# Performance work log

Measured on AMD Instinct MI355X. Metric: run time of the kernel, lower is better.

Reference implementation:

```python
import jax, jax.numpy as jnp
import numpy as np

# Dimensions inferred from the module (few-shot reweighted YOLOv2 region loss)
B, C, NA, NCPA = 64, 20, 5, 1          # batch, base classes, anchors, classes-per-anchor
H, W = 19, 19                           # feature map (608 input / stride 32)
T = 50                                  # cfg.max_boxes
THRESH = 0.6
COORD_SCALE = 1.0
CLASS_SCALE = 1.0
NB = B * C                              # per-class 'image' rows, as in the torch code
A4 = NA * H * W
EPS = 1e-12
BCE_EPS = 1e-7
ANCHORS = [[1.3221, 1.73145], [3.19275, 4.00944], [5.05587, 8.09892], [9.47112, 4.84053], [11.2364, 10.0071]]


def iou_xywh(x1, y1, w1, h1, x2, y2, w2, h2):
    # center-size IoU, matches darknet bbox_iou(x1y1x2y2=False)
    l = jnp.maximum(x1 - w1 * 0.5, x2 - w2 * 0.5)
    r = jnp.minimum(x1 + w1 * 0.5, x2 + w2 * 0.5)
    t = jnp.maximum(y1 - h1 * 0.5, y2 - h2 * 0.5)
    b = jnp.minimum(y1 + h1 * 0.5, y2 + h2 * 0.5)
    inter = jnp.clip(r - l, 0.0) * jnp.clip(b - t, 0.0)
    union = w1 * h1 + w2 * h2 - inter
    return inter / jnp.maximum(union, EPS)


def setup_inputs() -> dict:
    key = jax.random.key(0)
    k1, k2, k3, k4 = jax.random.split(key, 4)
    output = jax.random.normal(k1, (NB, NA * (5 + NCPA), H, W), jnp.float32) * 0.5
    # target rows: [cls, x, y, w, h] * T, coords in (0,1); x kept > 0 so all boxes are 'valid'
    cls_ids = jax.random.randint(k2, (B, C, T), 0, C).astype(jnp.float32)
    xy = jax.random.uniform(k3, (B, C, T, 2), minval=0.05, maxval=0.95)
    wh = jax.random.uniform(k4, (B, C, T, 2), minval=0.05, maxval=0.5)
    target = jnp.concatenate([cls_ids[..., None], xy, wh], axis=-1).reshape(B, C, T * 5)
    anchors = jnp.asarray(ANCHORS, jnp.float32)
    return {"output": output, "target": target, "anchors": anchors}


def _forward(output, target, anchors):
    target = jax.lax.stop_gradient(target)
    anchors = jax.lax.stop_gradient(anchors)
    out5 = output.reshape(NB, NA, 5 + NCPA, H, W)
    x = jax.nn.sigmoid(out5[:, :, 0])
    y = jax.nn.sigmoid(out5[:, :, 1])
    w = out5[:, :, 2]
    h = out5[:, :, 3]
    conf = jax.nn.sigmoid(out5[:, :, 4])
    # class logits regrouped to original batch: (B*NA*H*W, C)
    cls = out5[:, :, 5:5 + NCPA].reshape(NB, NA, H, W)
    cls_logits = cls.reshape(B, C, NA * H * W).transpose(0, 2, 1).reshape(-1, C)
    # decode pred boxes (detached, mirroring torch's use of .data)
    grid_x = jnp.arange(W, dtype=jnp.float32)[None, None, None, :]
    grid_y = jnp.arange(H, dtype=jnp.float32)[None, None, :, None]
    aw = anchors[:, 0][None, :, None, None]
    ah = anchors[:, 1][None, :, None, None]
    px = jax.lax.stop_gradient(x) + grid_x
    py = jax.lax.stop_gradient(y) + grid_y
    pw = jnp.exp(jax.lax.stop_gradient(w)) * aw
    ph = jnp.exp(jax.lax.stop_gradient(h)) * ah
    # ground-truth boxes per row
    tgt = target.reshape(NB, T, 5)
    cls_t = tgt[:, :, 0]
    gx = tgt[:, :, 1] * W
    gy = tgt[:, :, 2] * H
    gw = tgt[:, :, 3] * W
    gh = tgt[:, :, 4] * H
    # 'break on first zero x' semantics
    valid = jnp.cumprod((tgt[:, :, 1] != 0).astype(jnp.int32), axis=1) > 0
    # stage 1: zero conf_mask where any gt IoU > thresh (scan over T to avoid (NB,T,A4) blowup)
    pxf = px.reshape(NB, A4); pyf = py.reshape(NB, A4)
    pwf = pw.reshape(NB, A4); phf = ph.reshape(NB, A4)

    def iou_step(ci, xs):
        gxt, gyt, gwt, ght, vt = xs
        iou = iou_xywh(pxf, pyf, pwf, phf, gxt[:, None], gyt[:, None], gwt[:, None], ght[:, None])
        return jnp.maximum(ci, jnp.where(vt[:, None], iou, 0.0)), None

    cur_ious, _ = jax.lax.scan(iou_step, jnp.zeros((NB, A4), jnp.float32), (gx.T, gy.T, gw.T, gh.T, valid.T))
    conf_mask0 = jnp.where(cur_ious.reshape(NB, NA, H, W) > THRESH, 0.0, 1.0)
    # best anchor per gt by wh-only IoU
    inter = jnp.minimum(gw[..., None], anchors[:, 0]) * jnp.minimum(gh[..., None], anchors[:, 1])
    union = gw[..., None] * gh[..., None] + anchors[:, 0] * anchors[:, 1] - inter
    best_n = jnp.argmax(inter / jnp.maximum(union, EPS), axis=-1).astype(jnp.int32)  # (NB,T)
    gi = gx.astype(jnp.int32)
    gj = gy.astype(jnp.int32)
    # stage 2: ordered scatter of targets (later boxes overwrite earlier, as in the torch loops)
    binds = jnp.arange(NB)
    z = jnp.zeros((NB, NA, H, W), jnp.float32)
    # seen < 12800 branch: tx=ty=0.5, tw=th=0, coord_mask=1
    carry0 = (jnp.ones_like(z), z, conf_mask0, jnp.full_like(z, 0.5), jnp.full_like(z, 0.5), z, z, z, z)

    def tgt_step(carry, xs):
        cm, clm, cfm, tx, ty, tw, th, tconf, tcls = carry
        gxt, gyt, gwt, ght, bn, git, gjt, vt, ct = xs
        idx = (binds, bn, gjt, git)

        def upd(arr, val):
            return arr.at[idx].set(jnp.where(vt, val, arr[idx]))

        aw_b = anchors[bn, 0]
        ah_b = anchors[bn, 1]
        iou = iou_xywh(gxt, gyt, gwt, ght, px[idx], py[idx], pw[idx], ph[idx])
        cm = upd(cm, 1.0)
        clm = upd(clm, 1.0)
        cfm = upd(cfm, 1.0)
        tx = upd(tx, gxt - git.astype(jnp.float32))
        ty = upd(ty, gyt - gjt.astype(jnp.float32))
        tw = upd(tw, jnp.log(jnp.maximum(gwt, EPS) / aw_b))
        th = upd(th, jnp.log(jnp.maximum(ght, EPS) / ah_b))
        tconf = upd(tconf, iou)
        tcls = upd(tcls, ct)
        return (cm, clm, cfm, tx, ty, tw, th, tconf, tcls), None

    xs = (gx.T, gy.T, gw.T, gh.T, best_n.T, gi.T, gj.T, valid.T, cls_t.T)
    (coord_mask, cls_mask, conf_mask, tx, ty, tw, th, tconf, tcls), _ = jax.lax.scan(tgt_step, carry0, xs)
    # regroup per-class rows back to original batch (neg_ratio='full' -> counts[i] == C)
    cm_grp = cls_mask.reshape(B, C, NA, H, W).sum(axis=1)
    tcls_grp = tcls.reshape(B, C, NA, H, W).sum(axis=1)
    sel = (cm_grp == 1.0).reshape(-1)           # exclude colliding cells
    labels = tcls_grp.reshape(-1).astype(jnp.int32)

    def bce_mean(p, t):
        p = jnp.clip(p, BCE_EPS, 1.0 - BCE_EPS)
        return jnp.mean(-(t * jnp.log(p) + (1.0 - t) * jnp.log(1.0 - p)))

    loss_x = COORD_SCALE * bce_mean(x * coord_mask, tx * coord_mask)
    loss_y = COORD_SCALE * bce_mean(y * coord_mask, ty * coord_mask)
    loss_w = COORD_SCALE * 0.5 * jnp.mean((w * coord_mask - tw * coord_mask) ** 2)
    loss_h = COORD_SCALE * 0.5 * jnp.mean((h * coord_mask - th * coord_mask) ** 2)
    loss_conf = 0.5 * jnp.mean((conf * conf_mask - tconf * conf_mask) ** 2)
    logp = jax.nn.log_softmax(cls_logits, axis=-1)
    nll = -jnp.take_along_axis(logp, labels[:, None], axis=1)[:, 0]
    nsel = jnp.maximum(jnp.sum(sel.astype(jnp.float32)), 1.0)
    loss_cls = CLASS_SCALE * jnp.sum(jnp.where(sel, nll, 0.0)) / nsel
    return loss_x + loss_y + loss_w + loss_h + loss_conf + loss_cls


def reference(output, target, anchors):
    return _forward(output, target, anchors)
```

## Files before the change

kernel.cpp:

```cpp
#include <hip/hip_runtime.h>
#include <math.h>

constexpr int cB   = 64;
constexpr int cC   = 20;
constexpr int cNA  = 5;
constexpr int cH   = 19;
constexpr int cW   = 19;
constexpr int cT   = 50;
constexpr int cNB  = cB * cC;
constexpr int cHW  = cH * cW;
constexpr int cA4  = cNA * cHW;
constexpr int cCH  = cNA * 6;
constexpr long cNTOT = (long)cNB * cA4;
constexpr int cCLS_ROWS = cB * cA4;
constexpr int cCLS_BLOCKS = (cCLS_ROWS + 255) / 256;

constexpr int ACC_BANKS = 64;
constexpr int TGT_N   = cNB * cT;
constexpr size_t SZT   = (size_t)TGT_N * 4;
constexpr size_t OFF_CNT = 2560;
constexpr size_t OFF_GX  = 4096;
constexpr size_t OFF_GY  = OFF_GX  + SZT;
constexpr size_t OFF_GW  = OFF_GY  + SZT;
constexpr size_t OFF_GH  = OFF_GW  + SZT;
constexpr size_t OFF_CLS = OFF_GH  + SZT;
constexpr size_t OFF_HL  = OFF_CLS + SZT;
constexpr size_t OFF_HR  = OFF_HL  + SZT;
constexpr size_t OFF_HT  = OFF_HR  + SZT;
constexpr size_t OFF_HB  = OFF_HT  + SZT;
constexpr size_t OFF_HG  = OFF_HB  + SZT;
constexpr size_t OFF_WIN = OFF_HG  + SZT;

__device__ __forceinline__ float fexp(float x) {
    return __builtin_amdgcn_exp2f(x * 1.4426950408889634f);
}
__device__ __forceinline__ float flog(float x) {
    return __builtin_amdgcn_logf(x) * 0.6931471805599453f;
}
__device__ __forceinline__ float frcp(float x) { return __builtin_amdgcn_rcpf(x); }
__device__ __forceinline__ float fsigmoid(float x) { return frcp(1.0f + fexp(-x)); }

typedef _Float16 h2 __attribute__((ext_vector_type(2)));
union HU { unsigned u; h2 h; };
__device__ __forceinline__ unsigned splat2(float v) {
    HU x; _Float16 f = (_Float16)v; x.h[0] = f; x.h[1] = f; return x.u;
}

__global__ void k_prep(const float* __restrict__ target, const float* __restrict__ anch,
                       float* __restrict__ gx_, float* __restrict__ gy_,
                       float* __restrict__ gw_, float* __restrict__ gh_,
                       float* __restrict__ cls_,
                       unsigned* __restrict__ hl_, unsigned* __restrict__ hr_,
                       unsigned* __restrict__ ht_, unsigned* __restrict__ hb_,
                       unsigned* __restrict__ hg_,
                       int* __restrict__ winner, double* __restrict__ acc,
                       int* __restrict__ cnt) {
    const int nb = blockIdx.x;
    const int t  = threadIdx.x;
    if (nb == 0) {
        for (int k = t; k < 5 * ACC_BANKS; k += 64) acc[k] = 0.0;
        if (t == 0) *cnt = 0;
    }
    for (int k = t; k < cA4; k += 64) winner[(size_t)nb * cA4 + k] = -1;

    float cv = 0.f, xr = 1.f, yr = 0.f, wr = 0.f, hr = 0.f;
    if (t < cT) {
        const float* tg = target + (size_t)nb * (cT * 5) + t * 5;
        cv = tg[0]; xr = tg[1]; yr = tg[2]; wr = tg[3]; hr = tg[4];
    }
    unsigned long long nz = __ballot(xr != 0.0f);
    if (t < cT) {
        unsigned long long below = (t == 63) ? ~0ull : ((2ull << t) - 1ull);
        bool valid = ((~nz) & below) == 0ull;
        float gx = xr * (float)cW, gy = yr * (float)cH;
        float gw = wr * (float)cW, gh = hr * (float)cH;
        int o = nb * cT + t;
        gx_[o] = gx; gy_[o] = gy; gw_[o] = gw; gh_[o] = gh;
        cls_[o] = cv;
        if (valid) {
            hl_[o] = splat2(gx - 0.5f * gw);
            hr_[o] = splat2(gx + 0.5f * gw);
            ht_[o] = splat2(gy - 0.5f * gh);
            hb_[o] = splat2(gy + 0.5f * gh);
            hg_[o] = splat2(-0.6f * (gw * gh));
        } else {
            hl_[o] = splat2(1e30f);  hr_[o] = splat2(-1e30f);
            ht_[o] = splat2(1e30f);  hb_[o] = splat2(-1e30f);
            hg_[o] = splat2(0.0f);
        }
        float best = -1.0f; int bn = 0;
        for (int n = 0; n < cNA; ++n) {
            float aw = anch[2*n], ah = anch[2*n+1];
            float inter = fminf(gw, aw) * fminf(gh, ah);
            float uni   = gw*gh + aw*ah - inter;
            float r = inter / fmaxf(uni, 1e-12f);
            if (r > best) { best = r; bn = n; }
        }
        if (valid) {
            int gi = (int)gx, gj = (int)gy;
            atomicMax(&winner[(size_t)nb * cA4 + bn * cHW + gj * cW + gi], t);
        }
    }
    __syncthreads();
}

__launch_bounds__(256)
__global__ void k_main(const float* __restrict__ outp, const float* __restrict__ anch,
                       const float* __restrict__ gx_, const float* __restrict__ gy_,
                       const float* __restrict__ gw_, const float* __restrict__ gh_,
                       const unsigned* __restrict__ hl_, const unsigned* __restrict__ hr_,
                       const unsigned* __restrict__ ht_, const unsigned* __restrict__ hb_,
                       const unsigned* __restrict__ hg_,
                       const int* __restrict__ winner, double* __restrict__ acc) {
    __shared__ double s_red[3][4];
    const int tid  = threadIdx.x;
    const int nb   = blockIdx.x >> 1;
    const int base = ((blockIdx.x & 1) << 10) + tid;
    const int tb   = nb * cT;
    const float* obase = outp + (size_t)nb * (cCH * cHW);

    h2 pl2[2], pr2[2], pt2[2], pb2[2], ov2[2], pa06h[2];
    float conf[4], tcf[4];
    unsigned wbits = 0;
    float bce = 0.0f, sq = 0.0f;
    const h2 z2  = { (_Float16)0.0f, (_Float16)0.0f };
    const h2 c16 = { (_Float16)1.6f, (_Float16)1.6f };

    #pragma unroll
    for (int u = 0; u < 4; ++u) {
        int cell = base + (u << 8);
        bool a_  = cell < cA4;
        int cc   = a_ ? cell : (cA4 - 1);
        int na   = cc / cHW;
        int rem  = cc - na * cHW;
        int j    = rem / cW;
        int i    = rem - j * cW;
        const float* ob = obase + (size_t)(na * 6) * cHW + rem;
        float xl = ob[0], yl = ob[cHW], wl = ob[2*cHW], hl = ob[3*cHW], cl = ob[4*cHW];
        float aw = anch[2*na], ah = anch[2*na+1];
        float x  = fsigmoid(xl), y = fsigmoid(yl), cf = fsigmoid(cl);
        float px = x + (float)i, py = y + (float)j;
        float pw = fexp(wl) * aw, ph = fexp(hl) * ah;
        float l0 = px - 0.5f*pw, r0 = px + 0.5f*pw;
        float t0 = py - 0.5f*ph, b0 = py + 0.5f*ph;
        float pa = pw * ph;
        int p = u >> 1, s = u & 1;
        pl2[p][s] = (_Float16)l0;  pr2[p][s] = (_Float16)r0;
        pt2[p][s] = (_Float16)t0;  pb2[p][s] = (_Float16)b0;
        pa06h[p][s] = (_Float16)(0.6f * pa);
        ov2[p][s] = (_Float16)0.0f;
        conf[u] = cf; tcf[u] = 0.0f;

        float tx = 0.5f, ty = 0.5f, tw = 0.0f, th = 0.0f;
        int wt = winner[(size_t)nb * cA4 + cc];
        bool wfl = (wt >= 0) && a_;
        if (wfl) {
            wbits |= (1u << u);
            float gx = gx_[tb+wt], gy = gy_[tb+wt], gw = gw_[tb+wt], gh = gh_[tb+wt];
            tx = gx - (float)i; ty = gy - (float)j;
            tw = flog(fmaxf(gw, 1e-12f) * frcp(aw));
            th = flog(fmaxf(gh, 1e-12f) * frcp(ah));
            float iw = fminf(r0, gx + 0.5f*gw) - fmaxf(l0, gx - 0.5f*gw);
            float ih = fminf(b0, gy + 0.5f*gh) - fmaxf(t0, gy - 0.5f*gh);
            iw = fmaxf(iw, 0.0f); ih = fmaxf(ih, 0.0f);
            float inter = iw * ih;
            float uni   = gw*gh + pa - inter;
            tcf[u] = inter * frcp(fmaxf(uni, 1e-12f));
        }
        if (a_) {
            float pc = fminf(fmaxf(x, 1e-7f), 1.0f - 1e-7f);
            bce += -(tx * flog(pc) + (1.0f - tx) * flog(1.0f - pc));
            pc = fminf(fmaxf(y, 1e-7f), 1.0f - 1e-7f);
            bce += -(ty * flog(pc) + (1.0f - ty) * flog(1.0f - pc));
            float dw = wl - tw, dh = hl - th;
            sq += dw*dw + dh*dh;
        }
    }

    #pragma unroll 10
    for (int t = 0; t < cT; ++t) {
        HU a, b, c, d, e;
        a.u = hl_[tb + t]; b.u = hr_[tb + t];
        c.u = ht_[tb + t]; d.u = hb_[tb + t];
        e.u = hg_[tb + t];
        #pragma unroll
        for (int p = 0; p < 2; ++p) {
            h2 iw = __builtin_elementwise_min(pr2[p], b.h) - __builtin_elementwise_max(pl2[p], a.h);
            h2 ih = __builtin_elementwise_min(pb2[p], d.h) - __builtin_elementwise_max(pt2[p], c.h);
            iw = __builtin_elementwise_max(iw, z2);
            ih = __builtin_elementwise_max(ih, z2);
            ov2[p] = __builtin_elementwise_max(ov2[p], c16 * iw * ih + e.h);
        }
    }

    float sc = 0.0f;
    #pragma unroll
    for (int u = 0; u < 4; ++u) {
        int cell = base + (u << 8);
        if (cell >= cA4) continue;
        int p = u >> 1, s = u & 1;
        bool wfl  = (wbits >> u) & 1;
        bool over = ov2[p][s] > pa06h[p][s];
        float cm  = wfl ? 1.0f : (over ? 0.0f : 1.0f);
        float d   = (conf[u] - tcf[u]) * cm;
        sc += d * d;
    }

    double v0 = (double)bce, v1 = (double)sq, v2 = (double)sc;
    for (int off = 32; off > 0; off >>= 1) {
        v0 += __shfl_down(v0, off);
        v1 += __shfl_down(v1, off);
        v2 += __shfl_down(v2, off);
    }
    int lane = tid & 63, wid = tid >> 6;
    if (lane == 0) { s_red[0][wid] = v0; s_red[1][wid] = v1; s_red[2][wid] = v2; }
    __syncthreads();
    if (tid == 0) {
        double a0 = s_red[0][0] + s_red[0][1] + s_red[0][2] + s_red[0][3];
        double a1 = s_red[1][0] + s_red[1][1] + s_red[1][2] + s_red[1][3];
        double a2 = s_red[2][0] + s_red[2][1] + s_red[2][2] + s_red[2][3];
        int bank = blockIdx.x & (ACC_BANKS - 1);
        atomicAdd(&acc[0*ACC_BANKS + bank], a0);
        atomicAdd(&acc[1*ACC_BANKS + bank], a1);
        atomicAdd(&acc[2*ACC_BANKS + bank], a2);
    }
}

__launch_bounds__(256)
__global__ void k_cls(const float* __restrict__ outp, const float* __restrict__ cls_,
                      const int* __restrict__ winner, double* __restrict__ acc,
                      int* __restrict__ cnt, float* __restrict__ out) {
    __shared__ double s_red[2][4];
    __shared__ int s_last;
    int tid = threadIdx.x;
    int row = blockIdx.x * 256 + tid;
    double nll = 0.0, ns = 0.0;
    if (row < cCLS_ROWS) {
        int b = row / cA4;
        int a = row - b * cA4;
        int cnt1 = 0, selc = -1, selw = -1;
        #pragma unroll
        for (int c = 0; c < cC; ++c) {
            int wv = winner[(size_t)(b * cC + c) * cA4 + a];
            if (wv >= 0) { cnt1++; selc = c; selw = wv; }
        }
        if (cnt1 == 1) {
            int na  = a / cHW;
            int rem = a - na * cHW;
            const float* ob = outp + ((size_t)b * cC * cCH + na * 6 + 5) * cHW + rem;
            float l[cC]; float m = -1e30f;
            #pragma unroll
            for (int c = 0; c < cC; ++c) { l[c] = ob[(size_t)c * cCH * cHW]; m = fmaxf(m, l[c]); }
            float s = 0.0f;
            #pragma unroll
            for (int c = 0; c < cC; ++c) s += fexp(l[c] - m);
            int label = (int)cls_[(b * cC + selc) * cT + selw];
            nll = (double)(m + flog(s) - l[label]);
            ns  = 1.0;
        }
    }
    for (int off = 32; off > 0; off >>= 1) {
        nll += __shfl_down(nll, off);
        ns  += __shfl_down(ns, off);
    }
    int lane = tid & 63, wid = tid >> 6;
    if (lane == 0) { s_red[0][wid] = nll; s_red[1][wid] = ns; }
    __syncthreads();
    if (tid == 0) {
        double a0 = s_red[0][0] + s_red[0][1] + s_red[0][2] + s_red[0][3];
        double a1 = s_red[1][0] + s_red[1][1] + s_red[1][2] + s_red[1][3];
        int bank = blockIdx.x & (ACC_BANKS - 1);
        atomicAdd(&acc[3*ACC_BANKS + bank], a0);
        atomicAdd(&acc[4*ACC_BANKS + bank], a1);
        __threadfence();
        s_last = (atomicAdd(cnt, 1) == cCLS_BLOCKS - 1);
    }
    __syncthreads();
    if (s_last && tid < 64) {
        __threadfence();
        double s[5];
        #pragma unroll
        for (int j = 0; j < 5; ++j) {
            double v = atomicAdd(&acc[j * ACC_BANKS + tid], 0.0);
            for (int off = 32; off > 0; off >>= 1) v += __shfl_down(v, off);
            s[j] = v;
        }
        if (tid == 0) {
            double Ninv = 1.0 / (double)cNTOT;
            double loss = s[0] * Ninv
                        + 0.5 * s[1] * Ninv
                        + 0.5 * s[2] * Ninv
                        + s[3] / fmax(s[4], 1.0);
            out[0] = (float)loss;
        }
    }
}

extern "C" void kernel_launch(void* const* d_in, const int* in_sizes, int n_in,
                              void* d_out, int out_size, void* d_ws, size_t ws_size,
                              hipStream_t stream) {
    const float* output = (const float*)d_in[0];
    const float* target = (const float*)d_in[1];
    const float* anch   = (const float*)d_in[2];
    char* ws = (char*)d_ws;
    double*   acc  = (double*)ws;
    int*      cnt  = (int*)   (ws + OFF_CNT);
    float*    gx_  = (float*) (ws + OFF_GX);
    float*    gy_  = (float*) (ws + OFF_GY);
    float*    gw_  = (float*) (ws + OFF_GW);
    float*    gh_  = (float*) (ws + OFF_GH);
    float*    cls_ = (float*) (ws + OFF_CLS);
    unsigned* hl_  = (unsigned*)(ws + OFF_HL);
    unsigned* hr_  = (unsigned*)(ws + OFF_HR);
    unsigned* ht_  = (unsigned*)(ws + OFF_HT);
    unsigned* hb_  = (unsigned*)(ws + OFF_HB);
    unsigned* hg_  = (unsigned*)(ws + OFF_HG);
    int*      win  = (int*)   (ws + OFF_WIN);

    k_prep<<<cNB, 64, 0, stream>>>(target, anch, gx_, gy_, gw_, gh_, cls_,
                                   hl_, hr_, ht_, hb_, hg_, win, acc, cnt);
    k_main<<<cNB * 2, 256, 0, stream>>>(output, anch, gx_, gy_, gw_, gh_,
                                        hl_, hr_, ht_, hb_, hg_, win, acc);
    k_cls<<<cCLS_BLOCKS, 256, 0, stream>>>(output, cls_, win, acc, cnt, (float*)d_out);
}
```

Before: 141.3 us.

## Fuse target prep into main kernel with shared-memory winners and packed row encoding

Drops the separate prep kernel. Each main block now builds its ground-truth boxes and the winner map in shared memory, and processes one whole class-image (8 cells per thread) instead of half of one. Winning cells are packed into a per-batch row-encoding array with atomicAdd (count in the high bits, class and target index in the low bits). The class kernel therefore reads one int per row instead of 20 winner entries. This removes a launch and the global winner, box and gt arrays, at the cost of a memset, larger per-block work (half as many blocks) and more register pressure. The fp16 overlap check is rescaled by sqrt(1.6) instead of multiplying by 1.6.

```diff
diff --git a/kernel.cpp b/kernel.cpp
--- a/kernel.cpp
+++ b/kernel.cpp
@@ -16,20 +16,9 @@
 constexpr int cCLS_BLOCKS = (cCLS_ROWS + 255) / 256;
 
 constexpr int ACC_BANKS = 64;
-constexpr int TGT_N   = cNB * cT;
-constexpr size_t SZT   = (size_t)TGT_N * 4;
 constexpr size_t OFF_CNT = 2560;
-constexpr size_t OFF_GX  = 4096;
-constexpr size_t OFF_GY  = OFF_GX  + SZT;
-constexpr size_t OFF_GW  = OFF_GY  + SZT;
-constexpr size_t OFF_GH  = OFF_GW  + SZT;
-constexpr size_t OFF_CLS = OFF_GH  + SZT;
-constexpr size_t OFF_HL  = OFF_CLS + SZT;
-constexpr size_t OFF_HR  = OFF_HL  + SZT;
-constexpr size_t OFF_HT  = OFF_HR  + SZT;
-constexpr size_t OFF_HB  = OFF_HT  + SZT;
-constexpr size_t OFF_HG  = OFF_HB  + SZT;
-constexpr size_t OFF_WIN = OFF_HG  + SZT;
+constexpr size_t OFF_ROW = 4096;
+constexpr size_t ZERO_BYTES = OFF_ROW + (size_t)cB * cA4 * 4;
 
 __device__ __forceinline__ float fexp(float x) {
     return __builtin_amdgcn_exp2f(x * 1.4426950408889634f);
@@ -45,90 +34,94 @@
 __device__ __forceinline__ unsigned splat2(float v) {
     HU x; _Float16 f = (_Float16)v; x.h[0] = f; x.h[1] = f; return x.u;
 }
-
-__global__ void k_prep(const float* __restrict__ target, const float* __restrict__ anch,
-                       float* __restrict__ gx_, float* __restrict__ gy_,
-                       float* __restrict__ gw_, float* __restrict__ gh_,
-                       float* __restrict__ cls_,
-                       unsigned* __restrict__ hl_, unsigned* __restrict__ hr_,
-                       unsigned* __restrict__ ht_, unsigned* __restrict__ hb_,
-                       unsigned* __restrict__ hg_,
-                       int* __restrict__ winner, double* __restrict__ acc,
-                       int* __restrict__ cnt) {
-    const int nb = blockIdx.x;
-    const int t  = threadIdx.x;
-    if (nb == 0) {
-        for (int k = t; k < 5 * ACC_BANKS; k += 64) acc[k] = 0.0;
-        if (t == 0) *cnt = 0;
-    }
-    for (int k = t; k < cA4; k += 64) winner[(size_t)nb * cA4 + k] = -1;
-
-    float cv = 0.f, xr = 1.f, yr = 0.f, wr = 0.f, hr = 0.f;
-    if (t < cT) {
-        const float* tg = target + (size_t)nb * (cT * 5) + t * 5;
-        cv = tg[0]; xr = tg[1]; yr = tg[2]; wr = tg[3]; hr = tg[4];
-    }
-    unsigned long long nz = __ballot(xr != 0.0f);
-    if (t < cT) {
-        unsigned long long below = (t == 63) ? ~0ull : ((2ull << t) - 1ull);
-        bool valid = ((~nz) & below) == 0ull;
-        float gx = xr * (float)cW, gy = yr * (float)cH;
-        float gw = wr * (float)cW, gh = hr * (float)cH;
-        int o = nb * cT + t;
-        gx_[o] = gx; gy_[o] = gy; gw_[o] = gw; gh_[o] = gh;
-        cls_[o] = cv;
+constexpr float cS = 1.2649110640673518f;
+
+__launch_bounds__(256)
+__global__ void k_main(const float* __restrict__ outp, const float* __restrict__ target,
+                       const float* __restrict__ anch,
+                       int* __restrict__ rowenc, double* __restrict__ acc) {
+    __shared__ int s_win[cA4];
+    __shared__ __align__(16) unsigned s_box[cT][8];
+    __shared__ __align__(16) float4 s_gt[cT];
+    __shared__ double s_red[3][4];
+    const int tid = threadIdx.x;
+    const int nb  = blockIdx.x;
+    const int b_  = nb / cC;
+    const int c_  = nb - b_ * cC;
+    const float* obase = outp + (size_t)nb * (cCH * cHW);
+
+    for (int k = tid; k < cA4; k += 256) s_win[k] = -1;
+    __syncthreads();
+
+    if (tid < 64) {
+        const int t = tid;
+        float cv = 0.f, xr = 1.f, yr = 0.f, wr = 0.f, hr = 0.f;
+        if (t < cT) {
+            const float* tg = target + (size_t)nb * (cT * 5) + t * 5;
+            cv = tg[0]; xr = tg[1]; yr = tg[2]; wr = tg[3]; hr = tg[4];
+        }
+        (void)cv;
+        unsigned long long nz = __ballot(xr != 0.0f);
+        if (t < cT) {
+            unsigned long long below = (2ull << t) - 1ull;
+            bool valid = ((~nz) & below) == 0ull;
+            float gx = xr * (float)cW, gy = yr * (float)cH;
+            float gw = wr * (float)cW, gh = hr * (float)cH;
+            s_gt[t] = make_float4(gx, gy, gw, gh);
+            if (valid) {
+                s_box[t][0] = splat2(cS * (gx - 0.5f * gw));
+                s_box[t][1] = splat2(cS * (gx + 0.5f * gw));
+                s_box[t][2] = splat2(cS * (gy - 0.5f * gh));
+                s_box[t][3] = splat2(cS * (gy + 0.5f * gh));
+                s_box[t][4] = splat2(-0.6f * (gw * gh));
+            } else {
+                s_box[t][0] = splat2(1e4f);  s_box[t][1] = splat2(-1e4f);
+                s_box[t][2] = splat2(1e4f);  s_box[t][3] = splat2(-1e4f);
+                s_box[t][4] = splat2(0.0f);
+            }
+            if (valid) {
+                float best = -1.0f; int bn = 0;
+                for (int n = 0; n < cNA; ++n) {
+                    float aw = anch[2*n], ah = anch[2*n+1];
+                    float inter = fminf(gw, aw) * fminf(gh, ah);
+                    float uni   = gw*gh + aw*ah - inter;
+                    float r = inter / fmaxf(uni, 1e-12f);
+                    if (r > best) { best = r; bn = n; }
+                }
+                int cell = bn * cHW + (int)gy * cW + (int)gx;
+                atomicMax(&s_win[cell], t);
+            }
+        }
+    }
+    __syncthreads();
+    if (tid < cT) {
+        const float4 g = s_gt[tid];
+        HU hu; hu.u = s_box[tid][4];
+        bool valid = !((float)hu.h[0] == 0.0f && s_box[tid][1] == splat2(-1e4f));
         if (valid) {
-            hl_[o] = splat2(gx - 0.5f * gw);
-            hr_[o] = splat2(gx + 0.5f * gw);
-            ht_[o] = splat2(gy - 0.5f * gh);
-            hb_[o] = splat2(gy + 0.5f * gh);
-            hg_[o] = splat2(-0.6f * (gw * gh));
-        } else {
-            hl_[o] = splat2(1e30f);  hr_[o] = splat2(-1e30f);
-            ht_[o] = splat2(1e30f);  hb_[o] = splat2(-1e30f);
-            hg_[o] = splat2(0.0f);
-        }
-        float best = -1.0f; int bn = 0;
-        for (int n = 0; n < cNA; ++n) {
-            float aw = anch[2*n], ah = anch[2*n+1];
-            float inter = fminf(gw, aw) * fminf(gh, ah);
-            float uni   = gw*gh + aw*ah - inter;
-            float r = inter / fmaxf(uni, 1e-12f);
-            if (r > best) { best = r; bn = n; }
-        }
-        if (valid) {
-            int gi = (int)gx, gj = (int)gy;
-            atomicMax(&winner[(size_t)nb * cA4 + bn * cHW + gj * cW + gi], t);
-        }
-    }
-    __syncthreads();
-}
-
-__launch_bounds__(256)
-__global__ void k_main(const float* __restrict__ outp, const float* __restrict__ anch,
-                       const float* __restrict__ gx_, const float* __restrict__ gy_,
-                       const float* __restrict__ gw_, const float* __restrict__ gh_,
-                       const unsigned* __restrict__ hl_, const unsigned* __restrict__ hr_,
-                       const unsigned* __restrict__ ht_, const unsigned* __restrict__ hb_,
-                       const unsigned* __restrict__ hg_,
-                       const int* __restrict__ winner, double* __restrict__ acc) {
-    __shared__ double s_red[3][4];
-    const int tid  = threadIdx.x;
-    const int nb   = blockIdx.x >> 1;
-    const int base = ((blockIdx.x & 1) << 10) + tid;
-    const int tb   = nb * cT;
-    const float* obase = outp + (size_t)nb * (cCH * cHW);
-
-    h2 pl2[2], pr2[2], pt2[2], pb2[2], ov2[2], pa06h[2];
-    float conf[4], tcf[4];
+            float best = -1.0f; int bn = 0;
+            for (int n = 0; n < cNA; ++n) {
+                float aw = anch[2*n], ah = anch[2*n+1];
+                float inter = fminf(g.z, aw) * fminf(g.w, ah);
+                float uni   = g.z*g.w + aw*ah - inter;
+                float r = inter / fmaxf(uni, 1e-12f);
+                if (r > best) { best = r; bn = n; }
+            }
+            int cell = bn * cHW + (int)g.y * cW + (int)g.x;
+            if (s_win[cell] == tid)
+                atomicAdd(&rowenc[b_ * cA4 + cell], (1 << 10) | (c_ * cT + tid));
+        }
+    }
+
+    h2 pl2[4], pr2[4], pt2[4], pb2[4], ov2[4], pa06h[4];
+    float conf[8], tcf[8];
     unsigned wbits = 0;
     float bce = 0.0f, sq = 0.0f;
-    const h2 z2  = { (_Float16)0.0f, (_Float16)0.0f };
-    const h2 c16 = { (_Float16)1.6f, (_Float16)1.6f };
+    const h2 z2 = { (_Float16)0.0f, (_Float16)0.0f };
 
     #pragma unroll
-    for (int u = 0; u < 4; ++u) {
-        int cell = base + (u << 8);
+    for (int u = 0; u < 8; ++u) {
+        int cell = tid + (u << 8);
         bool a_  = cell < cA4;
         int cc   = a_ ? cell : (cA4 - 1);
         int na   = cc / cHW;
@@ -145,18 +138,19 @@
         float t0 = py - 0.5f*ph, b0 = py + 0.5f*ph;
         float pa = pw * ph;
         int p = u >> 1, s = u & 1;
-        pl2[p][s] = (_Float16)l0;  pr2[p][s] = (_Float16)r0;
-        pt2[p][s] = (_Float16)t0;  pb2[p][s] = (_Float16)b0;
+        pl2[p][s] = (_Float16)(cS * l0);  pr2[p][s] = (_Float16)(cS * r0);
+        pt2[p][s] = (_Float16)(cS * t0);  pb2[p][s] = (_Float16)(cS * b0);
         pa06h[p][s] = (_Float16)(0.6f * pa);
         ov2[p][s] = (_Float16)0.0f;
         conf[u] = cf; tcf[u] = 0.0f;
 
         float tx = 0.5f, ty = 0.5f, tw = 0.0f, th = 0.0f;
-        int wt = winner[(size_t)nb * cA4 + cc];
+        int wt = s_win[cc];
         bool wfl = (wt >= 0) && a_;
         if (wfl) {
             wbits |= (1u << u);
-            float gx = gx_[tb+wt], gy = gy_[tb+wt], gw = gw_[tb+wt], gh = gh_[tb+wt];
+            float4 g = s_gt[wt];
+            float gx = g.x, gy = g.y, gw = g.z, gh = g.w;
             tx = gx - (float)i; ty = gy - (float)j;
             tw = flog(fmaxf(gw, 1e-12f) * frcp(aw));
             th = flog(fmaxf(gh, 1e-12f) * frcp(ah));
@@ -179,24 +173,24 @@
 
     #pragma unroll 10
     for (int t = 0; t < cT; ++t) {
+        uint4 bx = *(const uint4*)&s_box[t][0];
+        unsigned gv = s_box[t][4];
         HU a, b, c, d, e;
-        a.u = hl_[tb + t]; b.u = hr_[tb + t];
-        c.u = ht_[tb + t]; d.u = hb_[tb + t];
-        e.u = hg_[tb + t];
+        a.u = bx.x; b.u = bx.y; c.u = bx.z; d.u = bx.w; e.u = gv;
         #pragma unroll
-        for (int p = 0; p < 2; ++p) {
+        for (int p = 0; p < 4; ++p) {
             h2 iw = __builtin_elementwise_min(pr2[p], b.h) - __builtin_elementwise_max(pl2[p], a.h);
             h2 ih = __builtin_elementwise_min(pb2[p], d.h) - __builtin_elementwise_max(pt2[p], c.h);
             iw = __builtin_elementwise_max(iw, z2);
             ih = __builtin_elementwise_max(ih, z2);
-            ov2[p] = __builtin_elementwise_max(ov2[p], c16 * iw * ih + e.h);
+            ov2[p] = __builtin_elementwise_max(ov2[p], iw * ih + e.h);
         }
     }
 
     float sc = 0.0f;
     #pragma unroll
-    for (int u = 0; u < 4; ++u) {
-        int cell = base + (u << 8);
+    for (int u = 0; u < 8; ++u) {
+        int cell = tid + (u << 8);
         if (cell >= cA4) continue;
         int p = u >> 1, s = u & 1;
         bool wfl  = (wbits >> u) & 1;
@@ -219,7 +213,7 @@
         double a0 = s_red[0][0] + s_red[0][1] + s_red[0][2] + s_red[0][3];
         double a1 = s_red[1][0] + s_red[1][1] + s_red[1][2] + s_red[1][3];
         double a2 = s_red[2][0] + s_red[2][1] + s_red[2][2] + s_red[2][3];
-        int bank = blockIdx.x & (ACC_BANKS - 1);
+        int bank = nb & (ACC_BANKS - 1);
         atomicAdd(&acc[0*ACC_BANKS + bank], a0);
         atomicAdd(&acc[1*ACC_BANKS + bank], a1);
         atomicAdd(&acc[2*ACC_BANKS + bank], a2);
@@ -227,8 +221,8 @@
 }
 
 __launch_bounds__(256)
-__global__ void k_cls(const float* __restrict__ outp, const float* __restrict__ cls_,
-                      const int* __restrict__ winner, double* __restrict__ acc,
+__global__ void k_cls(const float* __restrict__ outp, const float* __restrict__ target,
+                      const int* __restrict__ rowenc, double* __restrict__ acc,
                       int* __restrict__ cnt, float* __restrict__ out) {
     __shared__ double s_red[2][4];
     __shared__ int s_last;
@@ -236,15 +230,13 @@
     int row = blockIdx.x * 256 + tid;
     double nll = 0.0, ns = 0.0;
     if (row < cCLS_ROWS) {
-        int b = row / cA4;
-        int a = row - b * cA4;
-        int cnt1 = 0, selc = -1, selw = -1;
-        #pragma unroll
-        for (int c = 0; c < cC; ++c) {
-            int wv = winner[(size_t)(b * cC + c) * cA4 + a];
-            if (wv >= 0) { cnt1++; selc = c; selw = wv; }
-        }
-        if (cnt1 == 1) {
+        int v = rowenc[row];
+        if ((v >> 10) == 1) {
+            int payload = v & 1023;
+            int selc = payload / cT;
+            int selt = payload - selc * cT;
+            int b = row / cA4;
+            int a = row - b * cA4;
             int na  = a / cHW;
             int rem = a - na * cHW;
             const float* ob = outp + ((size_t)b * cC * cCH + na * 6 + 5) * cHW + rem;
@@ -254,7 +246,7 @@
             float s = 0.0f;
             #pragma unroll
             for (int c = 0; c < cC; ++c) s += fexp(l[c] - m);
-            int label = (int)cls_[(b * cC + selc) * cT + selw];
+            int label = (int)target[((size_t)(b * cC + selc) * cT + selt) * 5];
             nll = (double)(m + flog(s) - l[label]);
             ns  = 1.0;
         }
@@ -303,23 +295,12 @@
     const float* target = (const float*)d_in[1];
     const float* anch   = (const float*)d_in[2];
     char* ws = (char*)d_ws;
-    double*   acc  = (double*)ws;
-    int*      cnt  = (int*)   (ws + OFF_CNT);
-    float*    gx_  = (float*) (ws + OFF_GX);
-    float*    gy_  = (float*) (ws + OFF_GY);
-    float*    gw_  = (float*) (ws + OFF_GW);
-    float*    gh_  = (float*) (ws + OFF_GH);
-    float*    cls_ = (float*) (ws + OFF_CLS);
-    unsigned* hl_  = (unsigned*)(ws + OFF_HL);
-    unsigned* hr_  = (unsigned*)(ws + OFF_HR);
-    unsigned* ht_  = (unsigned*)(ws + OFF_HT);
-    unsigned* hb_  = (unsigned*)(ws + OFF_HB);
-    unsigned* hg_  = (unsigned*)(ws + OFF_HG);
-    int*      win  = (int*)   (ws + OFF_WIN);
-
-    k_prep<<<cNB, 64, 0, stream>>>(target, anch, gx_, gy_, gw_, gh_, cls_,
-                                   hl_, hr_, ht_, hb_, hg_, win, acc, cnt);
-    k_main<<<cNB * 2, 256, 0, stream>>>(output, anch, gx_, gy_, gw_, gh_,
-                                        hl_, hr_, ht_, hb_, hg_, win, acc);
-    k_cls<<<cCLS_BLOCKS, 256, 0, stream>>>(output, cls_, win, acc, cnt, (float*)d_out);
-}
+    double* acc    = (double*)ws;
+    int*    cnt    = (int*)(ws + OFF_CNT);
+    int*    rowenc = (int*)(ws + OFF_ROW);
+
+    hipMemsetAsync(ws, 0, ZERO_BYTES, stream);
+
+    k_main<<<cNB, 256, 0, stream>>>(output, target, anch, rowenc, acc);
+    k_cls<<<cCLS_BLOCKS, 256, 0, stream>>>(output, target, rowenc, acc, cnt, (float*)d_out);
+}
```

After: 131.2 us. 7.1% less time.
